# Optimization experiments

Measured on AMD Instinct MI355X. Metric: run time of the kernel, lower is better.

The kernel has to match this reference:

```python
import jax, jax.numpy as jnp
import numpy as np

N = 100000       # nodes
E = 1600000      # edges
V = 50000        # vocab
H = 256          # embedding dim (hsize)
A = 64           # per-head out dim (asize)
NH = 3           # num_heads
G = 64           # graphs in batch


def setup_inputs() -> dict:
    key = jax.random.key(0)
    ks = jax.random.split(key, 12)
    h0 = jax.random.randint(ks[0], (N,), 0, V)
    src = jax.random.randint(ks[1], (E,), 0, N)
    dst = jax.random.randint(ks[2], (E,), 0, N)
    graph_ids = jnp.sort(jax.random.randint(ks[3], (N,), 0, G))
    s = 0.05
    emb = jax.random.normal(ks[4], (V, H), jnp.float32) * s
    W_fc = jax.random.normal(ks[5], (H, NH * A), jnp.float32) * s   # GATConv fc
    attn_l = jax.random.normal(ks[6], (NH, A), jnp.float32) * s
    attn_r = jax.random.normal(ks[7], (NH, A), jnp.float32) * s
    bias_gat = jax.random.normal(ks[8], (NH, A), jnp.float32) * s
    W1 = jax.random.normal(ks[9], (A, 128), jnp.float32) * s
    b1 = jnp.zeros((128,), jnp.float32)
    W2 = jax.random.normal(ks[10], (128, 16), jnp.float32) * s
    b2 = jnp.zeros((16,), jnp.float32)
    return dict(h0=h0, src=src, dst=dst, graph_ids=graph_ids, emb=emb,
                W_fc=W_fc, attn_l=attn_l, attn_r=attn_r, bias_gat=bias_gat,
                W1=W1, b1=b1, W2=W2, b2=b2)


def reference(h0, src, dst, graph_ids, emb, W_fc, attn_l, attn_r, bias_gat,
              W1, b1, W2, b2):
    # embedding lookup
    h1 = emb[h0]                                            # [N, H]
    # GATConv: linear projection per head
    feat = (h1 @ W_fc).reshape(N, NH, A)                    # [N, NH, A]
    el = jnp.einsum('nha,ha->nh', feat, attn_l)             # [N, NH]
    er = jnp.einsum('nha,ha->nh', feat, attn_r)             # [N, NH]
    e = jax.nn.leaky_relu(el[src] + er[dst], 0.2)           # [E, NH]
    # segment softmax over incoming edges of each dst node
    m = jax.ops.segment_max(e, dst, num_segments=N)         # [N, NH]
    e_exp = jnp.exp(e - m[dst])                             # [E, NH]
    denom = jax.ops.segment_sum(e_exp, dst, num_segments=N) # [N, NH]
    alpha = e_exp / denom[dst]                              # [E, NH]
    # scatter-aggregate messages
    msg = alpha[:, :, None] * feat[src]                     # [E, NH, A]
    rst = jax.ops.segment_sum(msg, dst, num_segments=N)     # [N, NH, A]
    rst = rst + bias_gat[None]                              # GATConv bias
    # relu + mean over heads
    h2 = jnp.mean(jax.nn.relu(rst), axis=1)                 # [N, A]
    # MLP predictor: ReLU then Identity
    h3 = jax.nn.relu(h2 @ W1 + b1) @ W2 + b2                # [N, 16]
    # dgl.mean_nodes: per-graph mean readout
    sums = jax.ops.segment_sum(h3, graph_ids, num_segments=G)            # [G, 16]
    counts = jax.ops.segment_sum(jnp.ones((N,), h3.dtype), graph_ids, num_segments=G)
    return sums / jnp.maximum(counts, 1.0)[:, None]         # [G, 16]
```

## Files before the change

### kernel.cpp

```cpp
#include <hip/hip_runtime.h>
#include <hip/hip_bf16.h>

#define NNODES 100000
#define NEDGES 1600000
#define VOCAB 50000
#define HDIM 256
#define ADIM 64
#define NHEADS 3
#define FDIM 192
#define NGRAPH 64
#define NPART 64

typedef __attribute__((ext_vector_type(8))) short bf16x8;
typedef __attribute__((ext_vector_type(4))) float f32x4;

__device__ __forceinline__ float bf2f(unsigned short u) {
  return __uint_as_float((unsigned int)u << 16);
}
__device__ __forceinline__ unsigned short f2bf(float f) {
  unsigned int u = __float_as_uint(f);
  u += 0x7FFFu + ((u >> 16) & 1u);
  return (unsigned short)(u >> 16);
}

__global__ __launch_bounds__(256) void conv_weights_kernel(
    const float* __restrict__ Wfc, const float* __restrict__ W1,
    const float* __restrict__ W2, unsigned short* __restrict__ Wt,
    unsigned short* __restrict__ W1t, unsigned short* __restrict__ W2t)
{
  int i = blockIdx.x * 256 + threadIdx.x;
  if (i < HDIM * FDIM) {
    int c = i / HDIM, k = i % HDIM;
    Wt[i] = f2bf(Wfc[(size_t)k * FDIM + c]);
  } else if (i < HDIM * FDIM + 128 * 64) {
    int j = i - HDIM * FDIM;
    int c = j / 64, k = j % 64;
    W1t[j] = f2bf(W1[(size_t)k * 128 + c]);
  } else if (i < HDIM * FDIM + 128 * 64 + 16 * 128) {
    int j = i - HDIM * FDIM - 128 * 64;
    int c = j / 128, k = j % 128;
    W2t[j] = f2bf(W2[(size_t)k * 16 + c]);
  }
}

__global__ __launch_bounds__(256) void proj_gemm_kernel(
    const float* __restrict__ emb,
    const unsigned short* __restrict__ Wt,
    const float* __restrict__ attn_l,
    const float* __restrict__ attn_r,
    unsigned short* __restrict__ proj_bf,
    float4* __restrict__ elv4, float4* __restrict__ erv4, int V)
{
  const int wave = threadIdx.x >> 6;
  const int lane = threadIdx.x & 63;
  const int row0 = blockIdx.x * 64 + wave * 16;
  const int cb = lane & 15;
  const int q  = lane >> 4;
  int arow = row0 + cb;
  if (arow >= V) arow = V - 1;
  const int kgrp = q * 8;

  f32x4 acc[12];
#pragma unroll
  for (int c = 0; c < 12; ++c) acc[c] = (f32x4){0.f, 0.f, 0.f, 0.f};

  const float* arow_p = &emb[(size_t)arow * HDIM + kgrp];
  const unsigned short* bcol_p = &Wt[(size_t)cb * HDIM + kgrp];

#pragma unroll
  for (int ks = 0; ks < 8; ++ks) {
    float4 f0 = *reinterpret_cast<const float4*>(arow_p + ks * 32);
    float4 f1 = *reinterpret_cast<const float4*>(arow_p + ks * 32 + 4);
    bf16x8 a;
    a[0] = (short)f2bf(f0.x); a[1] = (short)f2bf(f0.y);
    a[2] = (short)f2bf(f0.z); a[3] = (short)f2bf(f0.w);
    a[4] = (short)f2bf(f1.x); a[5] = (short)f2bf(f1.y);
    a[6] = (short)f2bf(f1.z); a[7] = (short)f2bf(f1.w);
#pragma unroll
    for (int c = 0; c < 12; ++c) {
      bf16x8 b = *reinterpret_cast<const bf16x8*>(bcol_p + (size_t)c * 16 * HDIM + ks * 32);
      acc[c] = __builtin_amdgcn_mfma_f32_16x16x32_bf16(a, b, acc[c], 0, 0, 0);
    }
  }

  const int rb = row0 + 4 * q;
#pragma unroll
  for (int i = 0; i < 4; ++i) {
    int r = rb + i;
    if (r < V) {
#pragma unroll
      for (int c = 0; c < 12; ++c)
        proj_bf[(size_t)r * FDIM + c * 16 + cb] = f2bf(acc[c][i]);
    }
  }

  float al_v[12], ar_v[12];
#pragma unroll
  for (int c = 0; c < 12; ++c) {
    al_v[c] = attn_l[c * 16 + cb];
    ar_v[c] = attn_r[c * 16 + cb];
  }
  float elp[4][3], erp[4][3];
#pragma unroll
  for (int i = 0; i < 4; ++i)
#pragma unroll
    for (int h = 0; h < 3; ++h) {
      float sl = 0.f, sr = 0.f;
#pragma unroll
      for (int cc = 0; cc < 4; ++cc) {
        float v = acc[h * 4 + cc][i];
        sl += v * al_v[h * 4 + cc];
        sr += v * ar_v[h * 4 + cc];
      }
      elp[i][h] = sl; erp[i][h] = sr;
    }
#pragma unroll
  for (int s = 8; s > 0; s >>= 1) {
#pragma unroll
    for (int i = 0; i < 4; ++i)
#pragma unroll
      for (int h = 0; h < 3; ++h) {
        elp[i][h] += __shfl_xor(elp[i][h], s, 64);
        erp[i][h] += __shfl_xor(erp[i][h], s, 64);
      }
  }
  if (cb == 0) {
#pragma unroll
    for (int i = 0; i < 4; ++i) {
      int r = rb + i;
      if (r < V) {
        elv4[r] = make_float4(elp[i][0], elp[i][1], elp[i][2], 0.f);
        erv4[r] = make_float4(erp[i][0], erp[i][1], erp[i][2], 0.f);
      }
    }
  }
}

__global__ __launch_bounds__(256) void hist_kernel(
    const int* __restrict__ dst, int* __restrict__ cnt,
    unsigned short* __restrict__ rank16, int E)
{
  int e = blockIdx.x * 256 + threadIdx.x;
  if (e < E) rank16[e] = (unsigned short)atomicAdd(&cnt[dst[e]], 1);
}

__global__ __launch_bounds__(256) void scan_sum_kernel(
    const int* __restrict__ cnt, int* __restrict__ bsum, int n)
{
  __shared__ int red[256];
  int t = threadIdx.x;
  int base = blockIdx.x * 1024 + t * 4;
  int s = 0;
#pragma unroll
  for (int j = 0; j < 4; ++j) if (base + j < n) s += cnt[base + j];
  red[t] = s;
  __syncthreads();
  for (int o = 128; o > 0; o >>= 1) {
    if (t < o) red[t] += red[t + o];
    __syncthreads();
  }
  if (t == 0) bsum[blockIdx.x] = red[0];
}

__global__ void scan_bsum_kernel(int* bsum, int nb)
{
  if (threadIdx.x == 0 && blockIdx.x == 0) {
    int acc = 0;
    for (int i = 0; i < nb; ++i) { int v = bsum[i]; bsum[i] = acc; acc += v; }
  }
}

__global__ __launch_bounds__(256) void scan_write_kernel(
    const int* __restrict__ cnt, const int* __restrict__ bsum,
    int* __restrict__ offs, int n, int total)
{
  __shared__ int sd[256];
  int t = threadIdx.x;
  int base = blockIdx.x * 1024 + t * 4;
  int c[4];
  int ts = 0;
#pragma unroll
  for (int j = 0; j < 4; ++j) { c[j] = (base + j < n) ? cnt[base + j] : 0; ts += c[j]; }
  sd[t] = ts;
  __syncthreads();
  for (int o = 1; o < 256; o <<= 1) {
    int v = (t >= o) ? sd[t - o] : 0;
    __syncthreads();
    sd[t] += v;
    __syncthreads();
  }
  int run = sd[t] - ts + bsum[blockIdx.x];
#pragma unroll
  for (int j = 0; j < 4; ++j) {
    if (base + j < n) offs[base + j] = run;
    run += c[j];
  }
  if (blockIdx.x == 0 && t == 0) offs[n] = total;
}

__global__ __launch_bounds__(256) void scatter_kernel(
    const int* __restrict__ src, const int* __restrict__ dst,
    const int* __restrict__ h0, const unsigned short* __restrict__ rank16,
    const int* __restrict__ offs, unsigned short* __restrict__ recs16, int E)
{
  int e = blockIdx.x * 256 + threadIdx.x;
  if (e >= E) return;
  int p = offs[dst[e]] + (int)rank16[e];
  recs16[p] = (unsigned short)h0[src[e]];
}

__global__ __launch_bounds__(256) void wexp_kernel(
    const unsigned short* __restrict__ recs16, const int* __restrict__ offs,
    const int* __restrict__ h0,
    const float4* __restrict__ elv4, const float4* __restrict__ erv4,
    uint2* __restrict__ wrec, float4* __restrict__ inv4, int N)
{
  int n = blockIdx.x * 256 + threadIdx.x;
  if (n >= N) return;
  const float4 ero = erv4[h0[n]];
  int lo = offs[n], hi = offs[n + 1];
  float d0 = 0.f, d1 = 0.f, d2 = 0.f;
  for (int p = lo; p < hi; ++p) {
    unsigned v = recs16[p];
    float4 ev = elv4[v];
    float e0 = ev.x + ero.x, e1 = ev.y + ero.y, e2 = ev.z + ero.z;
    e0 = e0 > 0.f ? e0 : 0.2f * e0;
    e1 = e1 > 0.f ? e1 : 0.2f * e1;
    e2 = e2 > 0.f ? e2 : 0.2f * e2;
    unsigned short u0 = f2bf(__expf(e0));
    unsigned short u1 = f2bf(__expf(e1));
    unsigned short u2 = f2bf(__expf(e2));
    d0 += bf2f(u0); d1 += bf2f(u1); d2 += bf2f(u2);
    wrec[p] = make_uint2(v | ((unsigned)u0 << 16),
                         (unsigned)u1 | ((unsigned)u2 << 16));
  }
  inv4[n] = make_float4(d0 > 0.f ? 1.f / d0 : 0.f,
                        d1 > 0.f ? 1.f / d1 : 0.f,
                        d2 > 0.f ? 1.f / d2 : 0.f, 0.f);
}

__global__ __launch_bounds__(256) void aggregate_kernel(
    const uint2* __restrict__ wrec, const int* __restrict__ offs,
    const float4* __restrict__ inv4,
    const unsigned short* __restrict__ proj_bf, const float* __restrict__ bias_gat,
    unsigned short* __restrict__ h2bf, int N)
{
  int lane = threadIdx.x & 63;
  int n = blockIdx.x * 4 + (threadIdx.x >> 6);
  if (n >= N) return;
  int lo = offs[n], hi = offs[n + 1];
  float a0 = 0.f, a1 = 0.f, a2 = 0.f;

  int i = lo;
  for (; i + 4 <= hi; i += 4) {
    uint2 r[4];
#pragma unroll
    for (int j = 0; j < 4; ++j) r[j] = wrec[i + j];
    const unsigned short* ps[4];
#pragma unroll
    for (int j = 0; j < 4; ++j)
      ps[j] = &proj_bf[(size_t)(r[j].x & 0xFFFFu) * FDIM];
    float g0[4], g1[4], g2[4];
#pragma unroll
    for (int j = 0; j < 4; ++j) {
      g0[j] = bf2f(ps[j][lane]);
      g1[j] = bf2f(ps[j][64 + lane]);
      g2[j] = bf2f(ps[j][128 + lane]);
    }
#pragma unroll
    for (int j = 0; j < 4; ++j) {
      a0 += bf2f((unsigned short)(r[j].x >> 16)) * g0[j];
      a1 += bf2f((unsigned short)(r[j].y & 0xFFFFu)) * g1[j];
      a2 += bf2f((unsigned short)(r[j].y >> 16)) * g2[j];
    }
  }
  for (; i < hi; ++i) {
    uint2 r = wrec[i];
    const unsigned short* ps = &proj_bf[(size_t)(r.x & 0xFFFFu) * FDIM];
    a0 += bf2f((unsigned short)(r.x >> 16)) * bf2f(ps[lane]);
    a1 += bf2f((unsigned short)(r.y & 0xFFFFu)) * bf2f(ps[64 + lane]);
    a2 += bf2f((unsigned short)(r.y >> 16)) * bf2f(ps[128 + lane]);
  }

  const float4 inv = inv4[n];
  float r0 = a0 * inv.x + bias_gat[lane];
  float r1 = a1 * inv.y + bias_gat[64 + lane];
  float r2 = a2 * inv.z + bias_gat[128 + lane];
  float h2 = (fmaxf(r0, 0.f) + fmaxf(r1, 0.f) + fmaxf(r2, 0.f)) * (1.f / 3.f);
  h2bf[(size_t)n * 64 + lane] = f2bf(h2);
}

__global__ __launch_bounds__(256) void post_mfma_kernel(
    const unsigned short* __restrict__ h2bf,
    const unsigned short* __restrict__ W1t,
    const float* __restrict__ b1,
    const unsigned short* __restrict__ W2t,
    const float* __restrict__ b2, const int* __restrict__ gid,
    float* __restrict__ sums_priv, float* __restrict__ counts_priv, int N)
{
  __shared__ unsigned short z_lds[64 * 128];
  const int wave = threadIdx.x >> 6;
  const int lane = threadIdx.x & 63;
  const int r = lane & 15;
  const int q = lane >> 4;
  const int kg = q * 8;
  const int rw0 = blockIdx.x * 64 + wave * 16;

  int arow = rw0 + r;
  if (arow >= N) arow = N - 1;

  f32x4 acc1[8];
#pragma unroll
  for (int c = 0; c < 8; ++c) acc1[c] = (f32x4){0.f, 0.f, 0.f, 0.f};

#pragma unroll
  for (int ks = 0; ks < 2; ++ks) {
    bf16x8 a = *reinterpret_cast<const bf16x8*>(&h2bf[(size_t)arow * 64 + kg + ks * 32]);
#pragma unroll
    for (int c = 0; c < 8; ++c) {
      bf16x8 b = *reinterpret_cast<const bf16x8*>(&W1t[(size_t)(c * 16 + r) * 64 + kg + ks * 32]);
      acc1[c] = __builtin_amdgcn_mfma_f32_16x16x32_bf16(a, b, acc1[c], 0, 0, 0);
    }
  }
#pragma unroll
  for (int c = 0; c < 8; ++c) {
    float bb = b1[c * 16 + r];
#pragma unroll
    for (int i = 0; i < 4; ++i) {
      float z = acc1[c][i] + bb;
      z = z > 0.f ? z : 0.f;
      z_lds[(wave * 16 + 4 * q + i) * 128 + c * 16 + r] = f2bf(z);
    }
  }
  __syncthreads();

  f32x4 acc2 = (f32x4){0.f, 0.f, 0.f, 0.f};
#pragma unroll
  for (int ks = 0; ks < 4; ++ks) {
    bf16x8 a = *reinterpret_cast<const bf16x8*>(&z_lds[(wave * 16 + r) * 128 + kg + ks * 32]);
    bf16x8 b = *reinterpret_cast<const bf16x8*>(&W2t[(size_t)r * 128 + kg + ks * 32]);
    acc2 = __builtin_amdgcn_mfma_f32_16x16x32_bf16(a, b, acc2, 0, 0, 0);
  }
  const int part = blockIdx.x & (NPART - 1);
  float bb2 = b2[r];
#pragma unroll
  for (int i = 0; i < 4; ++i) {
    int row = rw0 + 4 * q + i;
    if (row < N) {
      int g = gid[row];
      atomicAdd(&sums_priv[(part * NGRAPH + g) * 16 + r], acc2[i] + bb2);
      if (r == 0) atomicAdd(&counts_priv[part * NGRAPH + g], 1.f);
    }
  }
}

__global__ void finalize_kernel(const float* __restrict__ sums_priv,
                                const float* __restrict__ counts_priv,
                                float* __restrict__ out)
{
  int j = threadIdx.x;
  int g = j >> 4;
  float s = 0.f, c = 0.f;
  for (int p = 0; p < NPART; ++p) {
    s += sums_priv[p * NGRAPH * 16 + j];
    c += counts_priv[p * NGRAPH + g];
  }
  out[j] = s / fmaxf(c, 1.f);
}

extern "C" void kernel_launch(void* const* d_in, const int* in_sizes, int n_in,
                              void* d_out, int out_size, void* d_ws, size_t ws_size,
                              hipStream_t stream)
{
  const int*   h0  = (const int*)  d_in[0];
  const int*   src = (const int*)  d_in[1];
  const int*   dst = (const int*)  d_in[2];
  const int*   gid = (const int*)  d_in[3];
  const float* emb = (const float*)d_in[4];
  const float* Wfc = (const float*)d_in[5];
  const float* al  = (const float*)d_in[6];
  const float* ar  = (const float*)d_in[7];
  const float* bg  = (const float*)d_in[8];
  const float* W1  = (const float*)d_in[9];
  const float* b1  = (const float*)d_in[10];
  const float* W2  = (const float*)d_in[11];
  const float* b2  = (const float*)d_in[12];
  float* out = (float*)d_out;

  char* ws = (char*)d_ws;
  size_t off = 0;
  auto alloc = [&](size_t bytes) -> void* {
    off = (off + 255) & ~(size_t)255;
    void* p = ws + off;
    off += bytes;
    return p;
  };
  unsigned short* Wt      = (unsigned short*)alloc((size_t)FDIM * HDIM * 2);
  unsigned short* W1t     = (unsigned short*)alloc((size_t)128 * 64 * 2);
  unsigned short* W2t     = (unsigned short*)alloc((size_t)16 * 128 * 2);
  unsigned short* proj_bf = (unsigned short*)alloc((size_t)VOCAB * FDIM * 2);
  unsigned short* h2bf    = (unsigned short*)alloc((size_t)NNODES * 64 * 2);
  unsigned short* recs16  = (unsigned short*)alloc((size_t)NEDGES * 2);
  unsigned short* rank16  = (unsigned short*)alloc((size_t)NEDGES * 2);
  uint2*  wrec   = (uint2*) alloc((size_t)NEDGES * 8);
  float4* elv4   = (float4*)alloc((size_t)VOCAB * 16);
  float4* erv4   = (float4*)alloc((size_t)VOCAB * 16);
  float4* inv4   = (float4*)alloc((size_t)NNODES * 16);
  int*    cnt    = (int*)   alloc((size_t)NNODES * 4);
  int*    offs   = (int*)   alloc((size_t)(NNODES + 1) * 4);
  int*    bsum   = (int*)   alloc((size_t)128 * 4);
  float*  sums   = (float*) alloc((size_t)NPART * NGRAPH * 16 * 4);
  float*  cnts   = (float*) alloc((size_t)NPART * NGRAPH * 4);

  hipMemsetAsync(cnt,  0, (size_t)NNODES * 4, stream);
  hipMemsetAsync(sums, 0, (size_t)NPART * NGRAPH * 16 * 4, stream);
  hipMemsetAsync(cnts, 0, (size_t)NPART * NGRAPH * 4, stream);

  const int NB = (NNODES + 1023) / 1024;

  conv_weights_kernel<<<(HDIM * FDIM + 128 * 64 + 16 * 128 + 255) / 256, 256, 0, stream>>>(
      Wfc, W1, W2, Wt, W1t, W2t);
  proj_gemm_kernel<<<(VOCAB + 63) / 64, 256, 0, stream>>>(emb, Wt, al, ar,
                                                          proj_bf, elv4, erv4, VOCAB);
  hist_kernel<<<(NEDGES + 255) / 256, 256, 0, stream>>>(dst, cnt, rank16, NEDGES);
  scan_sum_kernel<<<NB, 256, 0, stream>>>(cnt, bsum, NNODES);
  scan_bsum_kernel<<<1, 64, 0, stream>>>(bsum, NB);
  scan_write_kernel<<<NB, 256, 0, stream>>>(cnt, bsum, offs, NNODES, NEDGES);
  scatter_kernel<<<(NEDGES + 255) / 256, 256, 0, stream>>>(src, dst, h0, rank16, offs,
                                                           recs16, NEDGES);
  wexp_kernel<<<(NNODES + 255) / 256, 256, 0, stream>>>(recs16, offs, h0, elv4, erv4,
                                                        wrec, inv4, NNODES);
  aggregate_kernel<<<(NNODES + 3) / 4, 256, 0, stream>>>(wrec, offs, inv4, proj_bf,
                                                         bg, h2bf, NNODES);
  post_mfma_kernel<<<(NNODES + 63) / 64, 256, 0, stream>>>(h2bf, W1t, b1, W2t, b2, gid,
                                                           sums, cnts, NNODES);
  finalize_kernel<<<1, 1024, 0, stream>>>(sums, cnts, out);
}
```

Before: 346.9 us.

## Fuse pipeline kernels, single-block scan, wave-per-node softmax, fuse aggregate with MLP

Merges weight conversion with the degree histogram, and the projection GEMM with the edge scatter, by splitting each grid into two block roles. Replaces the three-kernel scan with one 1024-thread block and folds the three memsets into one. Changes wexp to one wave per node with a shuffle reduction. Fuses aggregation into the MLP kernel through a swizzled LDS tile so the h2 round trip to global memory disappears. The intent is to cut launch count and global traffic, at the cost of a serial single-block scan and lower parallelism in the fused aggregate loop.

```diff
diff --git a/kernel.cpp b/kernel.cpp
--- a/kernel.cpp
+++ b/kernel.cpp
@@ -11,6 +11,11 @@
 #define NGRAPH 64
 #define NPART 64
 
+#define CONV_ELEMS (HDIM * FDIM + 128 * 64 + 16 * 128)
+#define CONV_BLOCKS ((CONV_ELEMS + 255) / 256)
+#define HIST_BLOCKS ((NEDGES + 255) / 256)
+#define PROJ_BLOCKS ((VOCAB + 63) / 64)
+
 typedef __attribute__((ext_vector_type(8))) short bf16x8;
 typedef __attribute__((ext_vector_type(4))) float f32x4;
 
@@ -23,41 +28,85 @@
   return (unsigned short)(u >> 16);
 }
 
-__global__ __launch_bounds__(256) void conv_weights_kernel(
+__global__ __launch_bounds__(256) void conv_hist_kernel(
     const float* __restrict__ Wfc, const float* __restrict__ W1,
     const float* __restrict__ W2, unsigned short* __restrict__ Wt,
-    unsigned short* __restrict__ W1t, unsigned short* __restrict__ W2t)
-{
-  int i = blockIdx.x * 256 + threadIdx.x;
-  if (i < HDIM * FDIM) {
-    int c = i / HDIM, k = i % HDIM;
-    Wt[i] = f2bf(Wfc[(size_t)k * FDIM + c]);
-  } else if (i < HDIM * FDIM + 128 * 64) {
-    int j = i - HDIM * FDIM;
-    int c = j / 64, k = j % 64;
-    W1t[j] = f2bf(W1[(size_t)k * 128 + c]);
-  } else if (i < HDIM * FDIM + 128 * 64 + 16 * 128) {
-    int j = i - HDIM * FDIM - 128 * 64;
-    int c = j / 128, k = j % 128;
-    W2t[j] = f2bf(W2[(size_t)k * 16 + c]);
-  }
-}
-
-__global__ __launch_bounds__(256) void proj_gemm_kernel(
+    unsigned short* __restrict__ W1t, unsigned short* __restrict__ W2t,
+    const int* __restrict__ dst, int* __restrict__ cnt,
+    unsigned short* __restrict__ rank16)
+{
+  if (blockIdx.x < CONV_BLOCKS) {
+    int i = blockIdx.x * 256 + threadIdx.x;
+    if (i < HDIM * FDIM) {
+      int c = i / HDIM, k = i % HDIM;
+      Wt[i] = f2bf(Wfc[(size_t)k * FDIM + c]);
+    } else if (i < HDIM * FDIM + 128 * 64) {
+      int j = i - HDIM * FDIM;
+      int c = j / 64, k = j % 64;
+      W1t[j] = f2bf(W1[(size_t)k * 128 + c]);
+    } else if (i < CONV_ELEMS) {
+      int j = i - HDIM * FDIM - 128 * 64;
+      int c = j / 128, k = j % 128;
+      W2t[j] = f2bf(W2[(size_t)k * 16 + c]);
+    }
+  } else {
+    int e = (blockIdx.x - CONV_BLOCKS) * 256 + threadIdx.x;
+    if (e < NEDGES) rank16[e] = (unsigned short)atomicAdd(&cnt[dst[e]], 1);
+  }
+}
+
+__global__ __launch_bounds__(1024) void scan_fused_kernel(
+    const int* __restrict__ cnt, int* __restrict__ offs, int n)
+{
+  __shared__ int sd[1024];
+  const int C = 98;
+  int t = threadIdx.x;
+  int start = t * C, end = start + C;
+  if (start > n) start = n;
+  if (end > n) end = n;
+  int s = 0;
+  for (int i = start; i < end; ++i) s += cnt[i];
+  sd[t] = s;
+  __syncthreads();
+  for (int o = 1; o < 1024; o <<= 1) {
+    int v = (t >= o) ? sd[t - o] : 0;
+    __syncthreads();
+    sd[t] += v;
+    __syncthreads();
+  }
+  int run = sd[t] - s;
+  for (int i = start; i < end; ++i) {
+    offs[i] = run;
+    run += cnt[i];
+  }
+  if (t == 1023) offs[n] = run;
+}
+
+__global__ __launch_bounds__(256) void proj_scatter_kernel(
     const float* __restrict__ emb,
     const unsigned short* __restrict__ Wt,
-    const float* __restrict__ attn_l,
-    const float* __restrict__ attn_r,
+    const float* __restrict__ attn_l, const float* __restrict__ attn_r,
     unsigned short* __restrict__ proj_bf,
-    float4* __restrict__ elv4, float4* __restrict__ erv4, int V)
-{
+    float4* __restrict__ elv4, float4* __restrict__ erv4,
+    const int* __restrict__ src, const int* __restrict__ dst,
+    const int* __restrict__ h0, const unsigned short* __restrict__ rank16,
+    const int* __restrict__ offs, unsigned short* __restrict__ recs16)
+{
+  if (blockIdx.x >= PROJ_BLOCKS) {
+    int e = (blockIdx.x - PROJ_BLOCKS) * 256 + threadIdx.x;
+    if (e < NEDGES) {
+      int p = offs[dst[e]] + (int)rank16[e];
+      recs16[p] = (unsigned short)h0[src[e]];
+    }
+    return;
+  }
   const int wave = threadIdx.x >> 6;
   const int lane = threadIdx.x & 63;
   const int row0 = blockIdx.x * 64 + wave * 16;
   const int cb = lane & 15;
   const int q  = lane >> 4;
   int arow = row0 + cb;
-  if (arow >= V) arow = V - 1;
+  if (arow >= VOCAB) arow = VOCAB - 1;
   const int kgrp = q * 8;
 
   f32x4 acc[12];
@@ -87,7 +136,7 @@
 #pragma unroll
   for (int i = 0; i < 4; ++i) {
     int r = rb + i;
-    if (r < V) {
+    if (r < VOCAB) {
 #pragma unroll
       for (int c = 0; c < 12; ++c)
         proj_bf[(size_t)r * FDIM + c * 16 + cb] = f2bf(acc[c][i]);
@@ -128,85 +177,12 @@
 #pragma unroll
     for (int i = 0; i < 4; ++i) {
       int r = rb + i;
-      if (r < V) {
+      if (r < VOCAB) {
         elv4[r] = make_float4(elp[i][0], elp[i][1], elp[i][2], 0.f);
         erv4[r] = make_float4(erp[i][0], erp[i][1], erp[i][2], 0.f);
       }
     }
   }
-}
-
-__global__ __launch_bounds__(256) void hist_kernel(
-    const int* __restrict__ dst, int* __restrict__ cnt,
-    unsigned short* __restrict__ rank16, int E)
-{
-  int e = blockIdx.x * 256 + threadIdx.x;
-  if (e < E) rank16[e] = (unsigned short)atomicAdd(&cnt[dst[e]], 1);
-}
-
-__global__ __launch_bounds__(256) void scan_sum_kernel(
-    const int* __restrict__ cnt, int* __restrict__ bsum, int n)
-{
-  __shared__ int red[256];
-  int t = threadIdx.x;
-  int base = blockIdx.x * 1024 + t * 4;
-  int s = 0;
-#pragma unroll
-  for (int j = 0; j < 4; ++j) if (base + j < n) s += cnt[base + j];
-  red[t] = s;
-  __syncthreads();
-  for (int o = 128; o > 0; o >>= 1) {
-    if (t < o) red[t] += red[t + o];
-    __syncthreads();
-  }
-  if (t == 0) bsum[blockIdx.x] = red[0];
-}
-
-__global__ void scan_bsum_kernel(int* bsum, int nb)
-{
-  if (threadIdx.x == 0 && blockIdx.x == 0) {
-    int acc = 0;
-    for (int i = 0; i < nb; ++i) { int v = bsum[i]; bsum[i] = acc; acc += v; }
-  }
-}
-
-__global__ __launch_bounds__(256) void scan_write_kernel(
-    const int* __restrict__ cnt, const int* __restrict__ bsum,
-    int* __restrict__ offs, int n, int total)
-{
-  __shared__ int sd[256];
-  int t = threadIdx.x;
-  int base = blockIdx.x * 1024 + t * 4;
-  int c[4];
-  int ts = 0;
-#pragma unroll
-  for (int j = 0; j < 4; ++j) { c[j] = (base + j < n) ? cnt[base + j] : 0; ts += c[j]; }
-  sd[t] = ts;
-  __syncthreads();
-  for (int o = 1; o < 256; o <<= 1) {
-    int v = (t >= o) ? sd[t - o] : 0;
-    __syncthreads();
-    sd[t] += v;
-    __syncthreads();
-  }
-  int run = sd[t] - ts + bsum[blockIdx.x];
-#pragma unroll
-  for (int j = 0; j < 4; ++j) {
-    if (base + j < n) offs[base + j] = run;
-    run += c[j];
-  }
-  if (blockIdx.x == 0 && t == 0) offs[n] = total;
-}
-
-__global__ __launch_bounds__(256) void scatter_kernel(
-    const int* __restrict__ src, const int* __restrict__ dst,
-    const int* __restrict__ h0, const unsigned short* __restrict__ rank16,
-    const int* __restrict__ offs, unsigned short* __restrict__ recs16, int E)
-{
-  int e = blockIdx.x * 256 + threadIdx.x;
-  if (e >= E) return;
-  int p = offs[dst[e]] + (int)rank16[e];
-  recs16[p] = (unsigned short)h0[src[e]];
 }
 
 __global__ __launch_bounds__(256) void wexp_kernel(
@@ -215,13 +191,14 @@
     const float4* __restrict__ elv4, const float4* __restrict__ erv4,
     uint2* __restrict__ wrec, float4* __restrict__ inv4, int N)
 {
-  int n = blockIdx.x * 256 + threadIdx.x;
+  int lane = threadIdx.x & 63;
+  int n = blockIdx.x * 4 + (threadIdx.x >> 6);
   if (n >= N) return;
   const float4 ero = erv4[h0[n]];
   int lo = offs[n], hi = offs[n + 1];
   float d0 = 0.f, d1 = 0.f, d2 = 0.f;
-  for (int p = lo; p < hi; ++p) {
-    unsigned v = recs16[p];
+  for (int c = lo + lane; c < hi; c += 64) {
+    unsigned v = recs16[c];
     float4 ev = elv4[v];
     float e0 = ev.x + ero.x, e1 = ev.y + ero.y, e2 = ev.z + ero.z;
     e0 = e0 > 0.f ? e0 : 0.2f * e0;
@@ -231,83 +208,92 @@
     unsigned short u1 = f2bf(__expf(e1));
     unsigned short u2 = f2bf(__expf(e2));
     d0 += bf2f(u0); d1 += bf2f(u1); d2 += bf2f(u2);
-    wrec[p] = make_uint2(v | ((unsigned)u0 << 16),
+    wrec[c] = make_uint2(v | ((unsigned)u0 << 16),
                          (unsigned)u1 | ((unsigned)u2 << 16));
   }
-  inv4[n] = make_float4(d0 > 0.f ? 1.f / d0 : 0.f,
-                        d1 > 0.f ? 1.f / d1 : 0.f,
-                        d2 > 0.f ? 1.f / d2 : 0.f, 0.f);
-}
-
-__global__ __launch_bounds__(256) void aggregate_kernel(
+#pragma unroll
+  for (int s = 32; s > 0; s >>= 1) {
+    d0 += __shfl_xor(d0, s, 64);
+    d1 += __shfl_xor(d1, s, 64);
+    d2 += __shfl_xor(d2, s, 64);
+  }
+  if (lane == 0)
+    inv4[n] = make_float4(d0 > 0.f ? 1.f / d0 : 0.f,
+                          d1 > 0.f ? 1.f / d1 : 0.f,
+                          d2 > 0.f ? 1.f / d2 : 0.f, 0.f);
+}
+
+__global__ __launch_bounds__(256) void aggmlp_kernel(
     const uint2* __restrict__ wrec, const int* __restrict__ offs,
     const float4* __restrict__ inv4,
     const unsigned short* __restrict__ proj_bf, const float* __restrict__ bias_gat,
-    unsigned short* __restrict__ h2bf, int N)
-{
-  int lane = threadIdx.x & 63;
-  int n = blockIdx.x * 4 + (threadIdx.x >> 6);
-  if (n >= N) return;
-  int lo = offs[n], hi = offs[n + 1];
-  float a0 = 0.f, a1 = 0.f, a2 = 0.f;
-
-  int i = lo;
-  for (; i + 4 <= hi; i += 4) {
-    uint2 r[4];
-#pragma unroll
-    for (int j = 0; j < 4; ++j) r[j] = wrec[i + j];
-    const unsigned short* ps[4];
-#pragma unroll
-    for (int j = 0; j < 4; ++j)
-      ps[j] = &proj_bf[(size_t)(r[j].x & 0xFFFFu) * FDIM];
-    float g0[4], g1[4], g2[4];
-#pragma unroll
-    for (int j = 0; j < 4; ++j) {
-      g0[j] = bf2f(ps[j][lane]);
-      g1[j] = bf2f(ps[j][64 + lane]);
-      g2[j] = bf2f(ps[j][128 + lane]);
-    }
-#pragma unroll
-    for (int j = 0; j < 4; ++j) {
-      a0 += bf2f((unsigned short)(r[j].x >> 16)) * g0[j];
-      a1 += bf2f((unsigned short)(r[j].y & 0xFFFFu)) * g1[j];
-      a2 += bf2f((unsigned short)(r[j].y >> 16)) * g2[j];
-    }
-  }
-  for (; i < hi; ++i) {
-    uint2 r = wrec[i];
-    const unsigned short* ps = &proj_bf[(size_t)(r.x & 0xFFFFu) * FDIM];
-    a0 += bf2f((unsigned short)(r.x >> 16)) * bf2f(ps[lane]);
-    a1 += bf2f((unsigned short)(r.y & 0xFFFFu)) * bf2f(ps[64 + lane]);
-    a2 += bf2f((unsigned short)(r.y >> 16)) * bf2f(ps[128 + lane]);
-  }
-
-  const float4 inv = inv4[n];
-  float r0 = a0 * inv.x + bias_gat[lane];
-  float r1 = a1 * inv.y + bias_gat[64 + lane];
-  float r2 = a2 * inv.z + bias_gat[128 + lane];
-  float h2 = (fmaxf(r0, 0.f) + fmaxf(r1, 0.f) + fmaxf(r2, 0.f)) * (1.f / 3.f);
-  h2bf[(size_t)n * 64 + lane] = f2bf(h2);
-}
-
-__global__ __launch_bounds__(256) void post_mfma_kernel(
-    const unsigned short* __restrict__ h2bf,
     const unsigned short* __restrict__ W1t,
     const float* __restrict__ b1,
     const unsigned short* __restrict__ W2t,
     const float* __restrict__ b2, const int* __restrict__ gid,
     float* __restrict__ sums_priv, float* __restrict__ counts_priv, int N)
 {
+  __shared__ unsigned short h2s[64 * 64];
   __shared__ unsigned short z_lds[64 * 128];
+  char* h2b = (char*)h2s;
   const int wave = threadIdx.x >> 6;
   const int lane = threadIdx.x & 63;
+  const int base = blockIdx.x * 64;
+
+  float bg0 = bias_gat[lane], bg1 = bias_gat[64 + lane], bg2 = bias_gat[128 + lane];
+  for (int i = 0; i < 16; ++i) {
+    int ln = wave * 16 + i;
+    int n = base + ln;
+    float h2 = 0.f;
+    if (n < N) {
+      int lo = offs[n], hi = offs[n + 1];
+      float a0 = 0.f, a1 = 0.f, a2 = 0.f;
+      int idx = lo;
+      for (; idx + 8 <= hi; idx += 8) {
+        uint2 r[8];
+#pragma unroll
+        for (int t = 0; t < 8; ++t) r[t] = wrec[idx + t];
+        const unsigned short* ps[8];
+#pragma unroll
+        for (int t = 0; t < 8; ++t)
+          ps[t] = &proj_bf[(size_t)(r[t].x & 0xFFFFu) * FDIM];
+        float g0[8], g1[8], g2[8];
+#pragma unroll
+        for (int t = 0; t < 8; ++t) {
+          g0[t] = bf2f(ps[t][lane]);
+          g1[t] = bf2f(ps[t][64 + lane]);
+          g2[t] = bf2f(ps[t][128 + lane]);
+        }
+#pragma unroll
+        for (int t = 0; t < 8; ++t) {
+          a0 += bf2f((unsigned short)(r[t].x >> 16)) * g0[t];
+          a1 += bf2f((unsigned short)(r[t].y & 0xFFFFu)) * g1[t];
+          a2 += bf2f((unsigned short)(r[t].y >> 16)) * g2[t];
+        }
+      }
+      for (; idx < hi; ++idx) {
+        uint2 r = wrec[idx];
+        const unsigned short* ps = &proj_bf[(size_t)(r.x & 0xFFFFu) * FDIM];
+        a0 += bf2f((unsigned short)(r.x >> 16)) * bf2f(ps[lane]);
+        a1 += bf2f((unsigned short)(r.y & 0xFFFFu)) * bf2f(ps[64 + lane]);
+        a2 += bf2f((unsigned short)(r.y >> 16)) * bf2f(ps[128 + lane]);
+      }
+      const float4 inv = inv4[n];
+      float r0 = a0 * inv.x + bg0;
+      float r1 = a1 * inv.y + bg1;
+      float r2 = a2 * inv.z + bg2;
+      h2 = (fmaxf(r0, 0.f) + fmaxf(r1, 0.f) + fmaxf(r2, 0.f)) * (1.f / 3.f);
+    }
+    int byte = ln * 128 + lane * 2;
+    byte ^= (ln & 7) << 4;
+    *reinterpret_cast<unsigned short*>(h2b + byte) = f2bf(h2);
+  }
+  __syncthreads();
+
   const int r = lane & 15;
   const int q = lane >> 4;
   const int kg = q * 8;
-  const int rw0 = blockIdx.x * 64 + wave * 16;
-
-  int arow = rw0 + r;
-  if (arow >= N) arow = N - 1;
+  const int rw0 = base + wave * 16;
 
   f32x4 acc1[8];
 #pragma unroll
@@ -315,7 +301,9 @@
 
 #pragma unroll
   for (int ks = 0; ks < 2; ++ks) {
-    bf16x8 a = *reinterpret_cast<const bf16x8*>(&h2bf[(size_t)arow * 64 + kg + ks * 32]);
+    int abyte = (wave * 16 + r) * 128 + (kg + ks * 32) * 2;
+    abyte ^= (r & 7) << 4;
+    bf16x8 a = *reinterpret_cast<const bf16x8*>(h2b + abyte);
 #pragma unroll
     for (int c = 0; c < 8; ++c) {
       bf16x8 b = *reinterpret_cast<const bf16x8*>(&W1t[(size_t)(c * 16 + r) * 64 + kg + ks * 32]);
@@ -395,44 +383,38 @@
     off += bytes;
     return p;
   };
+  const size_t CNT_B  = (size_t)NNODES * 4;
+  const size_t CNT_BP = (CNT_B + 255) & ~(size_t)255;
+  const size_t SUMS_B = (size_t)NPART * NGRAPH * 16 * 4;
+  const size_t ZB     = CNT_BP + SUMS_B + (size_t)NPART * NGRAPH * 4;
+  char*  zero_base = (char*)alloc(ZB);
+  int*   cnt  = (int*)zero_base;
+  float* sums = (float*)(zero_base + CNT_BP);
+  float* cnts = (float*)(zero_base + CNT_BP + SUMS_B);
+
   unsigned short* Wt      = (unsigned short*)alloc((size_t)FDIM * HDIM * 2);
   unsigned short* W1t     = (unsigned short*)alloc((size_t)128 * 64 * 2);
   unsigned short* W2t     = (unsigned short*)alloc((size_t)16 * 128 * 2);
   unsigned short* proj_bf = (unsigned short*)alloc((size_t)VOCAB * FDIM * 2);
-  unsigned short* h2bf    = (unsigned short*)alloc((size_t)NNODES * 64 * 2);
   unsigned short* recs16  = (unsigned short*)alloc((size_t)NEDGES * 2);
   unsigned short* rank16  = (unsigned short*)alloc((size_t)NEDGES * 2);
   uint2*  wrec   = (uint2*) alloc((size_t)NEDGES * 8);
   float4* elv4   = (float4*)alloc((size_t)VOCAB * 16);
   float4* erv4   = (float4*)alloc((size_t)VOCAB * 16);
   float4* inv4   = (float4*)alloc((size_t)NNODES * 16);
-  int*    cnt    = (int*)   alloc((size_t)NNODES * 4);
   int*    offs   = (int*)   alloc((size_t)(NNODES + 1) * 4);
-  int*    bsum   = (int*)   alloc((size_t)128 * 4);
-  float*  sums   = (float*) alloc((size_t)NPART * NGRAPH * 16 * 4);
-  float*  cnts   = (float*) alloc((size_t)NPART * NGRAPH * 4);
-
-  hipMemsetAsync(cnt,  0, (size_t)NNODES * 4, stream);
-  hipMemsetAsync(sums, 0, (size_t)NPART * NGRAPH * 16 * 4, stream);
-  hipMemsetAsync(cnts, 0, (size_t)NPART * NGRAPH * 4, stream);
-
-  const int NB = (NNODES + 1023) / 1024;
-
-  conv_weights_kernel<<<(HDIM * FDIM + 128 * 64 + 16 * 128 + 255) / 256, 256, 0, stream>>>(
-      Wfc, W1, W2, Wt, W1t, W2t);
-  proj_gemm_kernel<<<(VOCAB + 63) / 64, 256, 0, stream>>>(emb, Wt, al, ar,
-                                                          proj_bf, elv4, erv4, VOCAB);
-  hist_kernel<<<(NEDGES + 255) / 256, 256, 0, stream>>>(dst, cnt, rank16, NEDGES);
-  scan_sum_kernel<<<NB, 256, 0, stream>>>(cnt, bsum, NNODES);
-  scan_bsum_kernel<<<1, 64, 0, stream>>>(bsum, NB);
-  scan_write_kernel<<<NB, 256, 0, stream>>>(cnt, bsum, offs, NNODES, NEDGES);
-  scatter_kernel<<<(NEDGES + 255) / 256, 256, 0, stream>>>(src, dst, h0, rank16, offs,
-                                                           recs16, NEDGES);
-  wexp_kernel<<<(NNODES + 255) / 256, 256, 0, stream>>>(recs16, offs, h0, elv4, erv4,
-                                                        wrec, inv4, NNODES);
-  aggregate_kernel<<<(NNODES + 3) / 4, 256, 0, stream>>>(wrec, offs, inv4, proj_bf,
-                                                         bg, h2bf, NNODES);
-  post_mfma_kernel<<<(NNODES + 63) / 64, 256, 0, stream>>>(h2bf, W1t, b1, W2t, b2, gid,
-                                                           sums, cnts, NNODES);
+
+  hipMemsetAsync(zero_base, 0, ZB, stream);
+
+  conv_hist_kernel<<<CONV_BLOCKS + HIST_BLOCKS, 256, 0, stream>>>(
+      Wfc, W1, W2, Wt, W1t, W2t, dst, cnt, rank16);
+  scan_fused_kernel<<<1, 1024, 0, stream>>>(cnt, offs, NNODES);
+  proj_scatter_kernel<<<PROJ_BLOCKS + HIST_BLOCKS, 256, 0, stream>>>(
+      emb, Wt, al, ar, proj_bf, elv4, erv4,
+      src, dst, h0, rank16, offs, recs16);
+  wexp_kernel<<<(NNODES + 3) / 4, 256, 0, stream>>>(recs16, offs, h0, elv4, erv4,
+                                                    wrec, inv4, NNODES);
+  aggmlp_kernel<<<(NNODES + 63) / 64, 256, 0, stream>>>(
+      wrec, offs, inv4, proj_bf, bg, W1t, b1, W2t, b2, gid, sums, cnts, NNODES);
   finalize_kernel<<<1, 1024, 0, stream>>>(sums, cnts, out);
 }
```

New measurement: 531.0 us. 1.53x slower.
